# Performance work log

Measured on AMD Instinct MI355X. Metric: run time of the kernel, lower is better.

## Reference

```python
import jax, jax.numpy as jnp
import numpy as np

HEADS = 4
HEAD_DIM = 64  # hidden_dim 256 / 4 heads
REG_W = 1e-05
EPS = 1e-08


def setup_inputs() -> dict:
    key = jax.random.key(0)
    ks = jax.random.split(key, 8)
    B, N, H, R = 4, 2048, 256, 8

    def xavier(k, shape):
        fan_in, fan_out = shape[-1], shape[-2]
        lim = jnp.sqrt(6.0 / (fan_in + fan_out))
        return jax.random.uniform(k, shape, jnp.float32, -lim, lim)

    return {
        "x": jax.random.normal(ks[0], (B, N, H), jnp.float32),
        "w_qkv_low": xavier(ks[1], (3 * R, H)),
        "b_qkv_low": jnp.zeros((3 * R,), jnp.float32),
        "w_qkv_high": xavier(ks[2], (3 * H, 3 * R)),
        "b_qkv_high": jnp.zeros((3 * H,), jnp.float32),
        "w_out_low": xavier(ks[3], (R, H)),
        "b_out_low": jnp.zeros((R,), jnp.float32),
        "w_out_high": xavier(ks[4], (H, R)),
        "b_out_high": jnp.zeros((H,), jnp.float32),
        "adj_u": xavier(ks[5], (HEADS, N, R)),
        "adj_v": xavier(ks[6], (HEADS, R, N)),
    }


def reference(x, w_qkv_low, b_qkv_low, w_qkv_high, b_qkv_high,
              w_out_low, b_out_low, w_out_high, b_out_high, adj_u, adj_v):
    B, N, H = x.shape
    # Low-rank factorized QKV projection
    qkv_low = x @ w_qkv_low.T + b_qkv_low            # [B, N, 3r]
    qkv = qkv_low @ w_qkv_high.T + b_qkv_high        # [B, N, 3H]
    q, k, v = jnp.split(qkv, 3, axis=-1)
    # [B, N, H] -> [B, heads, N, head_dim]
    def to_heads(t):
        return t.reshape(B, N, HEADS, HEAD_DIM).transpose(0, 2, 1, 3)
    q, k, v = to_heads(q), to_heads(k), to_heads(v)

    # Linearized attention with ELU+1 feature map (uses local copies of q,k)
    qf = jax.nn.elu(q) + 1.0
    kf = jax.nn.elu(k) + 1.0
    kv = jnp.einsum('bhnd,bhne->bhde', kf, v)        # [B, h, d, d]
    z = 1.0 / (kf.sum(-1) + EPS)                     # [B, h, N]
    out = jnp.einsum('bhnd,bhde,bhn->bhne', qf, kv, z)

    # Full softmax attention with low-rank adjacency bias (only its L1 mean is used)
    adj_bias = jnp.einsum('hnr,hrm->hnm', adj_u, adj_v)          # [h, N, N]
    scores = jnp.einsum('bhnd,bhmd->bhnm', q, k) / np.sqrt(HEAD_DIM)
    attn = jax.nn.softmax(scores + adj_bias, axis=-1)
    attn_reg_loss = REG_W * jnp.mean(jnp.abs(attn))

    # Merge heads and low-rank output projection
    out = out.transpose(0, 2, 1, 3).reshape(B, N, H)
    out = out @ w_out_low.T + b_out_low
    out = out @ w_out_high.T + b_out_high
    return out, attn_reg_loss
```

## Files before the change

kernel.cpp:

```cpp
#include <hip/hip_runtime.h>
#include <math.h>

#define B_     4
#define N_     2048
#define H_     256
#define ROWS   8192
#define EPS_   1e-8f
#define REGW   1e-5f
#define OUT_MAIN (ROWS*H_)

static __device__ __forceinline__ float elu1(float x) {
    return x > 0.f ? x + 1.f : __expf(x);
}

static __device__ __forceinline__ unsigned pack_bf16x2(float a, float b) {
    unsigned ua = __float_as_uint(a), ub = __float_as_uint(b);
    ua = (ua + 0x7FFFu + ((ua >> 16) & 1u)) >> 16;
    ub = (ub + 0x7FFFu + ((ub >> 16) & 1u)) & 0xFFFF0000u;
    return ua | ub;
}
static __device__ __forceinline__ float2 unpack_bf16x2(unsigned u) {
    return make_float2(__uint_as_float(u << 16), __uint_as_float(u & 0xFFFF0000u));
}

template<int MODE>
static __device__ __forceinline__ void chunk_compute(
    const float* __restrict__ buf, const float* __restrict__ qlT,
    const float* __restrict__ b_high, int chunk, size_t rowbase,
    int wv, int c, unsigned* __restrict__ outu, float* __restrict__ zg)
{
    float4 bh4 = *(const float4*)(b_high + chunk * 256 + c * 4);
    float4 a0 = bh4, a1 = bh4, a2 = bh4, a3 = bh4;
#pragma unroll
    for (int k = 0; k < 24; k++) {
        float4 w4 = *(const float4*)&buf[k * 260 + c * 4];
        float4 q4 = *(const float4*)&qlT[k * 16 + wv * 4];
        a0.x += q4.x * w4.x; a0.y += q4.x * w4.y; a0.z += q4.x * w4.z; a0.w += q4.x * w4.w;
        a1.x += q4.y * w4.x; a1.y += q4.y * w4.y; a1.z += q4.y * w4.z; a1.w += q4.y * w4.w;
        a2.x += q4.z * w4.x; a2.y += q4.z * w4.y; a2.z += q4.z * w4.z; a2.w += q4.z * w4.w;
        a3.x += q4.w * w4.x; a3.y += q4.w * w4.y; a3.z += q4.w * w4.z; a3.w += q4.w * w4.w;
    }
    const int h = c >> 4, dq = (c & 15) * 2;
    float4 aa[4] = {a0, a1, a2, a3};
    float zp[4];
#pragma unroll
    for (int rr = 0; rr < 4; rr++) {
        float4 a = aa[rr];
        if (MODE != 2) {
            a.x = elu1(a.x); a.y = elu1(a.y); a.z = elu1(a.z); a.w = elu1(a.w);
        }
        size_t row = rowbase + wv * 4 + rr;
        uint2 p;
        p.x = pack_bf16x2(a.x, a.y);
        p.y = pack_bf16x2(a.z, a.w);
        *(uint2*)(outu + ((size_t)h * ROWS + row) * 32 + dq) = p;
        if (MODE == 1) zp[rr] = a.x + a.y + a.z + a.w;
    }
    if (MODE == 1) {
#pragma unroll
        for (int rr = 0; rr < 4; rr++) {
            float s = zp[rr];
            s += __shfl_xor(s, 1, 16);
            s += __shfl_xor(s, 2, 16);
            s += __shfl_xor(s, 4, 16);
            s += __shfl_xor(s, 8, 16);
            zp[rr] = s;
        }
        if ((c & 15) == 0) {
#pragma unroll
            for (int rr = 0; rr < 4; rr++)
                zg[(rowbase + wv * 4 + rr) * 4 + h] = 1.f / (zp[rr] + EPS_);
        }
    }
}

static __device__ __forceinline__ void stage_whT(
    const float* __restrict__ wsrc, float* __restrict__ dst, int t)
{
#pragma unroll
    for (int i = 0; i < 6; i++) {
        int g = t + i * 256;
        float4 v4 = *(const float4*)(wsrc + g * 4);
        int e = g * 4, j = e / 24, k = e - j * 24;
        dst[(k + 0) * 260 + j] = v4.x;
        dst[(k + 1) * 260 + j] = v4.y;
        dst[(k + 2) * 260 + j] = v4.z;
        dst[(k + 3) * 260 + j] = v4.w;
    }
}

__global__ __launch_bounds__(256) void ka_fused(
    const float* __restrict__ x, const float* __restrict__ w_low,
    const float* __restrict__ b_low, const float* __restrict__ w_high,
    const float* __restrict__ b_high,
    unsigned* __restrict__ qf_u, unsigned* __restrict__ kf_u,
    unsigned* __restrict__ v_u, float* __restrict__ zg)
{
    __shared__ float bufA[24 * 260];
    __shared__ float bufB[24 * 260];
    __shared__ float qlT[24 * 16];

    const int t = threadIdx.x;
    const size_t rowbase = (size_t)blockIdx.x * 16;
    const int rb = t >> 4, c4 = t & 15;
    const int wv = t >> 6, c  = t & 63;

#pragma unroll
    for (int i = 0; i < 6; i++) {
        int g = t + i * 256;
        int j = g >> 6, k = (g & 63) * 4;
        *(float4*)&bufA[j * 260 + k] = *(const float4*)(w_low + g * 4);
    }
    stage_whT(w_high, bufB, t);
    float4 xr[4];
#pragma unroll
    for (int i = 0; i < 4; i++)
        xr[i] = *(const float4*)(x + (rowbase + rb) * H_ + i * 64 + c4 * 4);
    __syncthreads();

    {
        float ql[24];
#pragma unroll
        for (int j = 0; j < 24; j++) {
            float s = 0.f;
#pragma unroll
            for (int i = 0; i < 4; i++) {
                float4 w4 = *(const float4*)&bufA[j * 260 + i * 64 + c4 * 4];
                s += xr[i].x * w4.x + xr[i].y * w4.y + xr[i].z * w4.z + xr[i].w * w4.w;
            }
            s += __shfl_xor(s, 1, 16);
            s += __shfl_xor(s, 2, 16);
            s += __shfl_xor(s, 4, 16);
            s += __shfl_xor(s, 8, 16);
            ql[j] = s + b_low[j];
        }
        qlT[c4 * 16 + rb] = ql[c4];
        if (c4 < 8) qlT[(16 + c4) * 16 + rb] = ql[16 + c4];
    }
    __syncthreads();

    chunk_compute<0>(bufB, qlT, b_high, 0, rowbase, wv, c, qf_u, zg);
    stage_whT(w_high + 6144, bufA, t);
    __syncthreads();

    chunk_compute<1>(bufA, qlT, b_high, 1, rowbase, wv, c, kf_u, zg);
    stage_whT(w_high + 12288, bufB, t);
    __syncthreads();

    chunk_compute<2>(bufB, qlT, b_high, 2, rowbase, wv, c, v_u, zg);
}

__global__ __launch_bounds__(256) void k2_kv(
    const unsigned* __restrict__ kfu, const unsigned* __restrict__ vu,
    float* __restrict__ kvp)
{
    __shared__ float kfs[64 * 68];
    __shared__ float vss[64 * 68];
    const int blk = blockIdx.x;
    const int b = blk >> 7, h = (blk >> 5) & 3, ch = blk & 31;
    const int t = threadIdx.x;
    const size_t base_u = ((size_t)h * ROWS + (size_t)b * N_ + ch * 64) * 32;
#pragma unroll
    for (int i = 0; i < 2; i++) {
        int g = t + i * 256;
        int r = g >> 3, q = g & 7;
        uint4 ku = *(const uint4*)(kfu + base_u + r * 32 + q * 4);
        uint4 vv4 = *(const uint4*)(vu + base_u + r * 32 + q * 4);
        float2 f0 = unpack_bf16x2(ku.x), f1 = unpack_bf16x2(ku.y);
        float2 f2 = unpack_bf16x2(ku.z), f3 = unpack_bf16x2(ku.w);
        *(float4*)&kfs[r * 68 + q * 8 + 0] = make_float4(f0.x, f0.y, f1.x, f1.y);
        *(float4*)&kfs[r * 68 + q * 8 + 4] = make_float4(f2.x, f2.y, f3.x, f3.y);
        f0 = unpack_bf16x2(vv4.x); f1 = unpack_bf16x2(vv4.y);
        f2 = unpack_bf16x2(vv4.z); f3 = unpack_bf16x2(vv4.w);
        *(float4*)&vss[r * 68 + q * 8 + 0] = make_float4(f0.x, f0.y, f1.x, f1.y);
        *(float4*)&vss[r * 68 + q * 8 + 4] = make_float4(f2.x, f2.y, f3.x, f3.y);
    }
    __syncthreads();
    const int d0 = (t >> 4) * 4, e0 = (t & 15) * 4;
    float4 a0 = {0,0,0,0}, a1 = {0,0,0,0}, a2 = {0,0,0,0}, a3 = {0,0,0,0};
    for (int i = 0; i < 64; i++) {
        float4 kk = *(const float4*)&kfs[i * 68 + d0];
        float4 v4 = *(const float4*)&vss[i * 68 + e0];
        a0.x += kk.x * v4.x; a0.y += kk.x * v4.y; a0.z += kk.x * v4.z; a0.w += kk.x * v4.w;
        a1.x += kk.y * v4.x; a1.y += kk.y * v4.y; a1.z += kk.y * v4.z; a1.w += kk.y * v4.w;
        a2.x += kk.z * v4.x; a2.y += kk.z * v4.y; a2.z += kk.z * v4.z; a2.w += kk.z * v4.w;
        a3.x += kk.w * v4.x; a3.y += kk.w * v4.y; a3.z += kk.w * v4.z; a3.w += kk.w * v4.w;
    }
    float* outp = kvp + (size_t)blk * 4096;
    *(float4*)(outp + (d0 + 0) * 64 + e0) = a0;
    *(float4*)(outp + (d0 + 1) * 64 + e0) = a1;
    *(float4*)(outp + (d0 + 2) * 64 + e0) = a2;
    *(float4*)(outp + (d0 + 3) * 64 + e0) = a3;
}

__global__ __launch_bounds__(256) void k2b_reduce(
    const float* __restrict__ kvp, float* __restrict__ kvg,
    float* __restrict__ out)
{
    const int blk = blockIdx.x, t = threadIdx.x;
    const int bh = blk >> 4;
    const size_t pbase = (size_t)((bh >> 2) * 128 + (bh & 3) * 32);
    const int idx = (blk & 15) * 256 + t;
    float s = 0.f;
#pragma unroll 8
    for (int c = 0; c < 32; c++)
        s += kvp[(pbase + c) * 4096 + idx];
    kvg[(size_t)bh * 4096 + idx] = s;
    if (blk == 0 && t == 0)
        out[OUT_MAIN] = REGW / (float)N_;
}

__global__ __launch_bounds__(256) void k4_out(
    const unsigned* __restrict__ qfu, const float* __restrict__ zg,
    const float* __restrict__ kvg,
    const float* __restrict__ w_out_low, const float* __restrict__ b_out_low,
    const float* __restrict__ w_out_high, const float* __restrict__ b_out_high,
    float* __restrict__ out)
{
    __shared__ float qfs[16 * 260];
    __shared__ float lin[16 * 260];
    __shared__ float lows[16 * 8];
    __shared__ float zs[64];

    const int t = threadIdx.x, blk = blockIdx.x;
    const int rowbase = blk * 16;
    const int b = blk >> 7;
    const float* kvb = kvg + (size_t)b * 4 * 4096;

#pragma unroll
    for (int i = 0; i < 2; i++) {
        int g = t + i * 256;
        int h = g >> 7, rr = (g >> 3) & 15, q = g & 7;
        uint4 u = *(const uint4*)(qfu + ((size_t)h * ROWS + rowbase + rr) * 32 + q * 4);
        float2 f0 = unpack_bf16x2(u.x), f1 = unpack_bf16x2(u.y);
        float2 f2 = unpack_bf16x2(u.z), f3 = unpack_bf16x2(u.w);
        *(float4*)&qfs[rr * 260 + h * 64 + q * 8 + 0] = make_float4(f0.x, f0.y, f1.x, f1.y);
        *(float4*)&qfs[rr * 260 + h * 64 + q * 8 + 4] = make_float4(f2.x, f2.y, f3.x, f3.y);
    }
    if (t < 64) zs[t] = zg[(size_t)rowbase * 4 + t];
    __syncthreads();

    const int r = t >> 4, c4 = t & 15;
#pragma unroll
    for (int i = 0; i < 4; i++) {
        float4 acc = {0.f, 0.f, 0.f, 0.f};
        const float* kvh = kvb + i * 4096 + c4 * 4;
        for (int d4 = 0; d4 < 16; d4++) {
            float4 qa = *(const float4*)&qfs[r * 260 + i * 64 + d4 * 4];
            float4 k0 = *(const float4*)(kvh + (d4 * 4 + 0) * 64);
            float4 k1 = *(const float4*)(kvh + (d4 * 4 + 1) * 64);
            float4 k2 = *(const float4*)(kvh + (d4 * 4 + 2) * 64);
            float4 k3 = *(const float4*)(kvh + (d4 * 4 + 3) * 64);
            acc.x += qa.x * k0.x + qa.y * k1.x + qa.z * k2.x + qa.w * k3.x;
            acc.y += qa.x * k0.y + qa.y * k1.y + qa.z * k2.y + qa.w * k3.y;
            acc.z += qa.x * k0.z + qa.y * k1.z + qa.z * k2.z + qa.w * k3.z;
            acc.w += qa.x * k0.w + qa.y * k1.w + qa.z * k2.w + qa.w * k3.w;
        }
        float zv = zs[r * 4 + i];
        *(float4*)&lin[r * 260 + i * 64 + c4 * 4] =
            make_float4(acc.x * zv, acc.y * zv, acc.z * zv, acc.w * zv);
    }
    __syncthreads();

    if (t < 128) {
        int rr = t >> 3, j = t & 7;
        float a = b_out_low[j];
        const float4* wj = (const float4*)(w_out_low + j * H_);
#pragma unroll
        for (int kq = 0; kq < 64; kq++) {
            float4 l4 = *(const float4*)&lin[rr * 260 + kq * 4];
            float4 w4 = wj[kq];
            a += l4.x * w4.x + l4.y * w4.y + l4.z * w4.z + l4.w * w4.w;
        }
        lows[rr * 8 + j] = a;
    }
    __syncthreads();

    {
        int rr = t >> 4, ig = t & 15;
        float l[8];
#pragma unroll
        for (int j = 0; j < 8; j++) l[j] = lows[rr * 8 + j];
        float* outp = out + (size_t)(rowbase + rr) * H_;
#pragma unroll
        for (int i16 = 0; i16 < 4; i16++) {
            int i = i16 * 64 + ig * 4;
            const float* wh = w_out_high + i * 8;
            float4 s;
            s.x = b_out_high[i + 0]; s.y = b_out_high[i + 1];
            s.z = b_out_high[i + 2]; s.w = b_out_high[i + 3];
#pragma unroll
            for (int j = 0; j < 8; j++) {
                s.x += l[j] * wh[j];
                s.y += l[j] * wh[8 + j];
                s.z += l[j] * wh[16 + j];
                s.w += l[j] * wh[24 + j];
            }
            *(float4*)(outp + i) = s;
        }
    }
}

extern "C" void kernel_launch(void* const* d_in, const int* in_sizes, int n_in,
                              void* d_out, int out_size, void* d_ws, size_t ws_size,
                              hipStream_t stream) {
    const float* x          = (const float*)d_in[0];
    const float* w_qkv_low  = (const float*)d_in[1];
    const float* b_qkv_low  = (const float*)d_in[2];
    const float* w_qkv_high = (const float*)d_in[3];
    const float* b_qkv_high = (const float*)d_in[4];
    const float* w_out_low  = (const float*)d_in[5];
    const float* b_out_low  = (const float*)d_in[6];
    const float* w_out_high = (const float*)d_in[7];
    const float* b_out_high = (const float*)d_in[8];
    char* wsb = (char*)d_ws;
    unsigned* qf_u = (unsigned*)(wsb);
    unsigned* kf_u = (unsigned*)(wsb + ((size_t)4 << 20));
    unsigned* v_u  = (unsigned*)(wsb + ((size_t)8 << 20));
    float*    zg   = (float*)(wsb + ((size_t)12 << 20));
    float*    kvp  = (float*)(wsb + ((size_t)13 << 20));
    float*    kvg  = (float*)(wsb + ((size_t)21 << 20));
    float* out = (float*)d_out;

    ka_fused<<<512, 256, 0, stream>>>(x, w_qkv_low, b_qkv_low, w_qkv_high,
                                      b_qkv_high, qf_u, kf_u, v_u, zg);
    k2_kv<<<512, 256, 0, stream>>>(kf_u, v_u, kvp);
    k2b_reduce<<<256, 256, 0, stream>>>(kvp, kvg, out);
    k4_out<<<512, 256, 0, stream>>>(qf_u, zg, kvg, w_out_low, b_out_low,
                                    w_out_high, b_out_high, out);
}
```

Baseline: 140.8 us.

## Recompute Q features in output kernel from low-rank projection instead of storing bf16 Q

The first kernel stops computing and writing the bf16 Q features. It writes only the 24-wide low-rank projection, and the output kernel rebuilds elu(Q)+1 from it using w_qkv_high staged in shared memory. This cuts workspace write and read traffic, and Q is now kept in fp32 rather than bf16, in exchange for extra recomputation and more shared memory in k4_out. Separately, the KV partial kernel processes 128 rows per block instead of 64, halving its block count and the number of partials the reduce step has to sum.

```diff
diff --git a/kernel.cpp b/kernel.cpp
--- a/kernel.cpp
+++ b/kernel.cpp
@@ -21,57 +21,6 @@
 }
 static __device__ __forceinline__ float2 unpack_bf16x2(unsigned u) {
     return make_float2(__uint_as_float(u << 16), __uint_as_float(u & 0xFFFF0000u));
-}
-
-template<int MODE>
-static __device__ __forceinline__ void chunk_compute(
-    const float* __restrict__ buf, const float* __restrict__ qlT,
-    const float* __restrict__ b_high, int chunk, size_t rowbase,
-    int wv, int c, unsigned* __restrict__ outu, float* __restrict__ zg)
-{
-    float4 bh4 = *(const float4*)(b_high + chunk * 256 + c * 4);
-    float4 a0 = bh4, a1 = bh4, a2 = bh4, a3 = bh4;
-#pragma unroll
-    for (int k = 0; k < 24; k++) {
-        float4 w4 = *(const float4*)&buf[k * 260 + c * 4];
-        float4 q4 = *(const float4*)&qlT[k * 16 + wv * 4];
-        a0.x += q4.x * w4.x; a0.y += q4.x * w4.y; a0.z += q4.x * w4.z; a0.w += q4.x * w4.w;
-        a1.x += q4.y * w4.x; a1.y += q4.y * w4.y; a1.z += q4.y * w4.z; a1.w += q4.y * w4.w;
-        a2.x += q4.z * w4.x; a2.y += q4.z * w4.y; a2.z += q4.z * w4.z; a2.w += q4.z * w4.w;
-        a3.x += q4.w * w4.x; a3.y += q4.w * w4.y; a3.z += q4.w * w4.z; a3.w += q4.w * w4.w;
-    }
-    const int h = c >> 4, dq = (c & 15) * 2;
-    float4 aa[4] = {a0, a1, a2, a3};
-    float zp[4];
-#pragma unroll
-    for (int rr = 0; rr < 4; rr++) {
-        float4 a = aa[rr];
-        if (MODE != 2) {
-            a.x = elu1(a.x); a.y = elu1(a.y); a.z = elu1(a.z); a.w = elu1(a.w);
-        }
-        size_t row = rowbase + wv * 4 + rr;
-        uint2 p;
-        p.x = pack_bf16x2(a.x, a.y);
-        p.y = pack_bf16x2(a.z, a.w);
-        *(uint2*)(outu + ((size_t)h * ROWS + row) * 32 + dq) = p;
-        if (MODE == 1) zp[rr] = a.x + a.y + a.z + a.w;
-    }
-    if (MODE == 1) {
-#pragma unroll
-        for (int rr = 0; rr < 4; rr++) {
-            float s = zp[rr];
-            s += __shfl_xor(s, 1, 16);
-            s += __shfl_xor(s, 2, 16);
-            s += __shfl_xor(s, 4, 16);
-            s += __shfl_xor(s, 8, 16);
-            zp[rr] = s;
-        }
-        if ((c & 15) == 0) {
-#pragma unroll
-            for (int rr = 0; rr < 4; rr++)
-                zg[(rowbase + wv * 4 + rr) * 4 + h] = 1.f / (zp[rr] + EPS_);
-        }
-    }
 }
 
 static __device__ __forceinline__ void stage_whT(
@@ -89,12 +38,64 @@
     }
 }
 
+template<int MODE>
+static __device__ __forceinline__ void chunk_compute(
+    const float* __restrict__ buf, const float* __restrict__ qlT,
+    const float* __restrict__ b_high, size_t rowbase,
+    int wv, int c, unsigned* __restrict__ outu, float* __restrict__ zg)
+{
+    const int chunk = (MODE == 1) ? 1 : 2;
+    float4 bh4 = *(const float4*)(b_high + chunk * 256 + c * 4);
+    float4 a0 = bh4, a1 = bh4, a2 = bh4, a3 = bh4;
+#pragma unroll
+    for (int k = 0; k < 24; k++) {
+        float4 w4 = *(const float4*)&buf[k * 260 + c * 4];
+        float4 q4 = *(const float4*)&qlT[k * 16 + wv * 4];
+        a0.x += q4.x * w4.x; a0.y += q4.x * w4.y; a0.z += q4.x * w4.z; a0.w += q4.x * w4.w;
+        a1.x += q4.y * w4.x; a1.y += q4.y * w4.y; a1.z += q4.y * w4.z; a1.w += q4.y * w4.w;
+        a2.x += q4.z * w4.x; a2.y += q4.z * w4.y; a2.z += q4.z * w4.z; a2.w += q4.z * w4.w;
+        a3.x += q4.w * w4.x; a3.y += q4.w * w4.y; a3.z += q4.w * w4.z; a3.w += q4.w * w4.w;
+    }
+    const int h = c >> 4, dq = (c & 15) * 2;
+    float4 aa[4] = {a0, a1, a2, a3};
+    float zp[4];
+#pragma unroll
+    for (int rr = 0; rr < 4; rr++) {
+        float4 a = aa[rr];
+        if (MODE == 1) {
+            a.x = elu1(a.x); a.y = elu1(a.y); a.z = elu1(a.z); a.w = elu1(a.w);
+        }
+        size_t row = rowbase + wv * 4 + rr;
+        uint2 p;
+        p.x = pack_bf16x2(a.x, a.y);
+        p.y = pack_bf16x2(a.z, a.w);
+        *(uint2*)(outu + ((size_t)h * ROWS + row) * 32 + dq) = p;
+        if (MODE == 1) zp[rr] = a.x + a.y + a.z + a.w;
+    }
+    if (MODE == 1) {
+#pragma unroll
+        for (int rr = 0; rr < 4; rr++) {
+            float s = zp[rr];
+            s += __shfl_xor(s, 1, 16);
+            s += __shfl_xor(s, 2, 16);
+            s += __shfl_xor(s, 4, 16);
+            s += __shfl_xor(s, 8, 16);
+            zp[rr] = s;
+        }
+        if ((c & 15) == 0) {
+#pragma unroll
+            for (int rr = 0; rr < 4; rr++)
+                zg[(rowbase + wv * 4 + rr) * 4 + h] = 1.f / (zp[rr] + EPS_);
+        }
+    }
+}
+
 __global__ __launch_bounds__(256) void ka_fused(
     const float* __restrict__ x, const float* __restrict__ w_low,
     const float* __restrict__ b_low, const float* __restrict__ w_high,
-    const float* __restrict__ b_high,
-    unsigned* __restrict__ qf_u, unsigned* __restrict__ kf_u,
-    unsigned* __restrict__ v_u, float* __restrict__ zg)
+    const float* __restrict__ b_high, float* __restrict__ g_ql,
+    unsigned* __restrict__ kf_u, unsigned* __restrict__ v_u,
+    float* __restrict__ zg)
 {
     __shared__ float bufA[24 * 260];
     __shared__ float bufB[24 * 260];
@@ -111,7 +112,7 @@
         int j = g >> 6, k = (g & 63) * 4;
         *(float4*)&bufA[j * 260 + k] = *(const float4*)(w_low + g * 4);
     }
-    stage_whT(w_high, bufB, t);
+    stage_whT(w_high + 6144, bufB, t);
     float4 xr[4];
 #pragma unroll
     for (int i = 0; i < 4; i++)
@@ -134,34 +135,33 @@
             s += __shfl_xor(s, 8, 16);
             ql[j] = s + b_low[j];
         }
+        size_t row = rowbase + rb;
+        g_ql[(size_t)c4 * ROWS + row] = ql[c4];
+        if (c4 < 8) g_ql[(size_t)(16 + c4) * ROWS + row] = ql[16 + c4];
         qlT[c4 * 16 + rb] = ql[c4];
         if (c4 < 8) qlT[(16 + c4) * 16 + rb] = ql[16 + c4];
     }
     __syncthreads();
 
-    chunk_compute<0>(bufB, qlT, b_high, 0, rowbase, wv, c, qf_u, zg);
-    stage_whT(w_high + 6144, bufA, t);
-    __syncthreads();
-
-    chunk_compute<1>(bufA, qlT, b_high, 1, rowbase, wv, c, kf_u, zg);
-    stage_whT(w_high + 12288, bufB, t);
-    __syncthreads();
-
-    chunk_compute<2>(bufB, qlT, b_high, 2, rowbase, wv, c, v_u, zg);
+    stage_whT(w_high + 12288, bufA, t);
+    chunk_compute<1>(bufB, qlT, b_high, rowbase, wv, c, kf_u, zg);
+    __syncthreads();
+
+    chunk_compute<2>(bufA, qlT, b_high, rowbase, wv, c, v_u, zg);
 }
 
 __global__ __launch_bounds__(256) void k2_kv(
     const unsigned* __restrict__ kfu, const unsigned* __restrict__ vu,
     float* __restrict__ kvp)
 {
-    __shared__ float kfs[64 * 68];
-    __shared__ float vss[64 * 68];
+    __shared__ float kfs[128 * 68];
+    __shared__ float vss[128 * 68];
     const int blk = blockIdx.x;
-    const int b = blk >> 7, h = (blk >> 5) & 3, ch = blk & 31;
+    const int b = blk >> 6, h = (blk >> 4) & 3, ch = blk & 15;
     const int t = threadIdx.x;
-    const size_t base_u = ((size_t)h * ROWS + (size_t)b * N_ + ch * 64) * 32;
-#pragma unroll
-    for (int i = 0; i < 2; i++) {
+    const size_t base_u = ((size_t)h * ROWS + (size_t)b * N_ + ch * 128) * 32;
+#pragma unroll
+    for (int i = 0; i < 4; i++) {
         int g = t + i * 256;
         int r = g >> 3, q = g & 7;
         uint4 ku = *(const uint4*)(kfu + base_u + r * 32 + q * 4);
@@ -178,7 +178,7 @@
     __syncthreads();
     const int d0 = (t >> 4) * 4, e0 = (t & 15) * 4;
     float4 a0 = {0,0,0,0}, a1 = {0,0,0,0}, a2 = {0,0,0,0}, a3 = {0,0,0,0};
-    for (int i = 0; i < 64; i++) {
+    for (int i = 0; i < 128; i++) {
         float4 kk = *(const float4*)&kfs[i * 68 + d0];
         float4 v4 = *(const float4*)&vss[i * 68 + e0];
         a0.x += kk.x * v4.x; a0.y += kk.x * v4.y; a0.z += kk.x * v4.z; a0.w += kk.x * v4.w;
@@ -199,11 +199,11 @@
 {
     const int blk = blockIdx.x, t = threadIdx.x;
     const int bh = blk >> 4;
-    const size_t pbase = (size_t)((bh >> 2) * 128 + (bh & 3) * 32);
+    const size_t pbase = (size_t)((bh >> 2) * 64 + (bh & 3) * 16);
     const int idx = (blk & 15) * 256 + t;
     float s = 0.f;
-#pragma unroll 8
-    for (int c = 0; c < 32; c++)
+#pragma unroll
+    for (int c = 0; c < 16; c++)
         s += kvp[(pbase + c) * 4096 + idx];
     kvg[(size_t)bh * 4096 + idx] = s;
     if (blk == 0 && t == 0)
@@ -211,14 +211,17 @@
 }
 
 __global__ __launch_bounds__(256) void k4_out(
-    const unsigned* __restrict__ qfu, const float* __restrict__ zg,
+    const float* __restrict__ g_ql, const float* __restrict__ w_high,
+    const float* __restrict__ b_high, const float* __restrict__ zg,
     const float* __restrict__ kvg,
     const float* __restrict__ w_out_low, const float* __restrict__ b_out_low,
     const float* __restrict__ w_out_high, const float* __restrict__ b_out_high,
     float* __restrict__ out)
 {
+    __shared__ float bufW[24 * 260];
     __shared__ float qfs[16 * 260];
     __shared__ float lin[16 * 260];
+    __shared__ float qlT[24 * 16];
     __shared__ float lows[16 * 8];
     __shared__ float zs[64];
 
@@ -227,17 +230,40 @@
     const int b = blk >> 7;
     const float* kvb = kvg + (size_t)b * 4 * 4096;
 
-#pragma unroll
-    for (int i = 0; i < 2; i++) {
-        int g = t + i * 256;
-        int h = g >> 7, rr = (g >> 3) & 15, q = g & 7;
-        uint4 u = *(const uint4*)(qfu + ((size_t)h * ROWS + rowbase + rr) * 32 + q * 4);
-        float2 f0 = unpack_bf16x2(u.x), f1 = unpack_bf16x2(u.y);
-        float2 f2 = unpack_bf16x2(u.z), f3 = unpack_bf16x2(u.w);
-        *(float4*)&qfs[rr * 260 + h * 64 + q * 8 + 0] = make_float4(f0.x, f0.y, f1.x, f1.y);
-        *(float4*)&qfs[rr * 260 + h * 64 + q * 8 + 4] = make_float4(f2.x, f2.y, f3.x, f3.y);
+    stage_whT(w_high, bufW, t);
+    {
+        int k = t >> 4, r = t & 15;
+        qlT[t] = g_ql[(size_t)k * ROWS + rowbase + r];
+        if (t < 128) {
+            int idx2 = 256 + t;
+            int k2 = idx2 >> 4, r2 = idx2 & 15;
+            qlT[idx2] = g_ql[(size_t)k2 * ROWS + rowbase + r2];
+        }
     }
     if (t < 64) zs[t] = zg[(size_t)rowbase * 4 + t];
+    __syncthreads();
+
+    {
+        const int wv = t >> 6, c = t & 63;
+        float4 bh4 = *(const float4*)(b_high + c * 4);
+        float4 a0 = bh4, a1 = bh4, a2 = bh4, a3 = bh4;
+#pragma unroll
+        for (int k = 0; k < 24; k++) {
+            float4 w4 = *(const float4*)&bufW[k * 260 + c * 4];
+            float4 q4 = *(const float4*)&qlT[k * 16 + wv * 4];
+            a0.x += q4.x * w4.x; a0.y += q4.x * w4.y; a0.z += q4.x * w4.z; a0.w += q4.x * w4.w;
+            a1.x += q4.y * w4.x; a1.y += q4.y * w4.y; a1.z += q4.y * w4.z; a1.w += q4.y * w4.w;
+            a2.x += q4.z * w4.x; a2.y += q4.z * w4.y; a2.z += q4.z * w4.z; a2.w += q4.z * w4.w;
+            a3.x += q4.w * w4.x; a3.y += q4.w * w4.y; a3.z += q4.w * w4.z; a3.w += q4.w * w4.w;
+        }
+        float4 aa[4] = {a0, a1, a2, a3};
+#pragma unroll
+        for (int rr = 0; rr < 4; rr++) {
+            float4 a = aa[rr];
+            a.x = elu1(a.x); a.y = elu1(a.y); a.z = elu1(a.z); a.w = elu1(a.w);
+            *(float4*)&qfs[(wv * 4 + rr) * 260 + c * 4] = a;
+        }
+    }
     __syncthreads();
 
     const int r = t >> 4, c4 = t & 15;
@@ -314,18 +340,19 @@
     const float* w_out_high = (const float*)d_in[7];
     const float* b_out_high = (const float*)d_in[8];
     char* wsb = (char*)d_ws;
-    unsigned* qf_u = (unsigned*)(wsb);
-    unsigned* kf_u = (unsigned*)(wsb + ((size_t)4 << 20));
-    unsigned* v_u  = (unsigned*)(wsb + ((size_t)8 << 20));
-    float*    zg   = (float*)(wsb + ((size_t)12 << 20));
-    float*    kvp  = (float*)(wsb + ((size_t)13 << 20));
-    float*    kvg  = (float*)(wsb + ((size_t)21 << 20));
+    float*    g_ql = (float*)(wsb);
+    unsigned* kf_u = (unsigned*)(wsb + ((size_t)1 << 20));
+    unsigned* v_u  = (unsigned*)(wsb + ((size_t)5 << 20));
+    float*    zg   = (float*)(wsb + ((size_t)9 << 20));
+    float*    kvp  = (float*)(wsb + ((size_t)10 << 20));
+    float*    kvg  = (float*)(wsb + ((size_t)14 << 20));
     float* out = (float*)d_out;
 
     ka_fused<<<512, 256, 0, stream>>>(x, w_qkv_low, b_qkv_low, w_qkv_high,
-                                      b_qkv_high, qf_u, kf_u, v_u, zg);
-    k2_kv<<<512, 256, 0, stream>>>(kf_u, v_u, kvp);
+                                      b_qkv_high, g_ql, kf_u, v_u, zg);
+    k2_kv<<<256, 256, 0, stream>>>(kf_u, v_u, kvp);
     k2b_reduce<<<256, 256, 0, stream>>>(kvp, kvg, out);
-    k4_out<<<512, 256, 0, stream>>>(qf_u, zg, kvg, w_out_low, b_out_low,
-                                    w_out_high, b_out_high, out);
-}
+    k4_out<<<512, 256, 0, stream>>>(g_ql, w_qkv_high, b_qkv_high, zg, kvg,
+                                    w_out_low, b_out_low, w_out_high,
+                                    b_out_high, out);
+}
```

After: 136.9 us. 2.8% less time.
